# Performance work log

Hardware: AMD Instinct MI355X
Metric: run time of the kernel (lower is better)

Reference implementation:

```python
import jax, jax.numpy as jnp
import numpy as np

N_NODES = 100000
N_EDGES = 300000
D_IN = 256
D_OUT = 256


def setup_inputs() -> dict:
    key = jax.random.key(0)
    k1, k2, k3 = jax.random.split(key, 3)
    z = jax.random.normal(k1, (N_NODES, D_IN), dtype=jnp.float32)
    edge_index = jax.random.randint(k2, (2, N_EDGES), 0, N_NODES, dtype=jnp.int64)
    # Linear(input_dim, out_dim): weight [out, in], stored transposed for x @ W
    W = jax.random.normal(k3, (D_IN, D_OUT), dtype=jnp.float32) / np.sqrt(D_IN)
    b = jnp.zeros((D_OUT,), dtype=jnp.float32)
    return {"z": z, "edge_index": edge_index, "W": W, "b": b}


def reference(z, edge_index, W, b):
    # h = Linear(z): [N, D_out]
    h = z @ W + b
    # gather endpoint embeddings and take per-edge dot product
    src = h[edge_index[0]]  # [E, D_out]
    dst = h[edge_index[1]]  # [E, D_out]
    value = jnp.sum(src * dst, axis=1)  # [E]
    return jax.nn.sigmoid(value)
```

## Files before the change

kernel.cpp:

```cpp
#include <hip/hip_runtime.h>
#include <hip/hip_bf16.h>
#include <hip/hip_fp16.h>
#include <math.h>


#define D_DIM 256
#define BM 64

typedef __attribute__((ext_vector_type(8))) _Float16 half8;
typedef __attribute__((ext_vector_type(4))) float f32x4;

__device__ half8 g_Wf[8 * 256 * 4];

__global__ __launch_bounds__(256) void pack_w_kernel(const float* __restrict__ W) {
  int t = blockIdx.x * 256 + threadIdx.x;
  int kb = t >> 10;
  int qd = (t >> 8) & 3;
  int n  = t & 255;
  half8 o;
#pragma unroll
  for (int j = 0; j < 8; j++)
    o[j] = (_Float16)W[(size_t)(kb * 32 + qd * 8 + j) * D_DIM + n];
  g_Wf[(kb * 256 + n) * 4 + qd] = o;
}

__device__ inline void stage_b(int kb, char* buf, int wv, int lane) {
  const char* gsrc = (const char*)g_Wf + (size_t)kb * 16384 + wv * 2048;
  char* ldst = buf + wv * 2048;
#pragma unroll
  for (int i = 0; i < 2; i++) {
    __builtin_amdgcn_global_load_lds(
        (const __attribute__((address_space(1))) void*)(gsrc + i * 1024 + lane * 16),
        (__attribute__((address_space(3))) void*)(ldst + i * 1024),
        16, 0, 0);
  }
}

__global__ __launch_bounds__(512) void gemm_mfma_kernel(
    const float* __restrict__ z, const float* __restrict__ b,
    __half* __restrict__ h, int nrows) {
  __shared__ char smem[34816];
  const int tid = threadIdx.x;
  const int lane = tid & 63;
  const int wv = tid >> 6;
  const int mg = wv >> 1;
  const int nh = wv & 1;
  const int fr = lane & 15;
  const int qd = lane >> 4;
  const int row0 = blockIdx.x * BM + mg * 16;

  f32x4 acc[8];
#pragma unroll
  for (int j = 0; j < 8; j++) acc[j] = (f32x4)0.f;

  int r = row0 + fr;
  r = r < nrows ? r : (nrows - 1);
  const float* zrow = z + (size_t)r * D_DIM + qd * 8;

  float4 a0[2], a1[2];

  stage_b(0, smem, wv, lane);
  a0[0] = *(const float4*)(zrow);
  a1[0] = *(const float4*)(zrow + 4);
  __syncthreads();

#pragma unroll
  for (int kb = 0; kb < 8; kb++) {
    const int cA = kb & 1;
    const int nA = cA ^ 1;
    char* cur = smem + (kb & 1) * 16384;

    if (kb < 7) {
      stage_b(kb + 1, smem + ((kb + 1) & 1) * 16384, wv, lane);
      const float* p = zrow + (kb + 1) * 32;
      a0[nA] = *(const float4*)(p);
      a1[nA] = *(const float4*)(p + 4);
    }

    half8 af;
    af[0] = (_Float16)a0[cA].x; af[1] = (_Float16)a0[cA].y;
    af[2] = (_Float16)a0[cA].z; af[3] = (_Float16)a0[cA].w;
    af[4] = (_Float16)a1[cA].x; af[5] = (_Float16)a1[cA].y;
    af[6] = (_Float16)a1[cA].z; af[7] = (_Float16)a1[cA].w;

    const half8* buf = (const half8*)cur;
#pragma unroll
    for (int fn = 0; fn < 8; fn++) {
      int fi = (nh * 128 + fn * 16 + fr) * 4 + qd;
      half8 bf = buf[fi];
      acc[fn] = __builtin_amdgcn_mfma_f32_16x16x32_f16(af, bf, acc[fn], 0, 0, 0);
    }

    __syncthreads();
  }

  __half* et = (__half*)(smem + wv * 4352);
  float bias[8];
#pragma unroll
  for (int fn = 0; fn < 8; fn++) bias[fn] = b[nh * 128 + fn * 16 + fr];

#pragma unroll
  for (int fn = 0; fn < 8; fn++)
#pragma unroll
    for (int rr = 0; rr < 4; rr++)
      et[(qd * 4 + rr) * 136 + fn * 16 + fr] = __float2half(acc[fn][rr] + bias[fn]);
#pragma unroll
  for (int p = 0; p < 4; p++) {
    int idx = p * 64 + lane;
    int rr = idx >> 4;
    int cc = idx & 15;
    float4 v = *(const float4*)(et + rr * 136 + cc * 8);
    int row = row0 + rr;
    if (row < nrows)
      *(float4*)(h + (size_t)row * D_DIM + nh * 128 + cc * 8) = v;
  }
}

__global__ __launch_bounds__(256) void edge_dot_kernel(
    const int* __restrict__ ei, const __half* __restrict__ h,
    float* __restrict__ out, int E) {
  int wid = (blockIdx.x * blockDim.x + threadIdx.x) >> 6;
  int lane = threadIdx.x & 63;
  int ebase = wid * 8;
  if (ebase >= E) return;
  const int half = lane >> 5;
  const int off = lane & 31;

  float4 v[8];
#pragma unroll
  for (int q = 0; q < 8; q++) {
    int e = ebase + q;
    e = e < E ? e : (E - 1);
    int node = half ? ei[E + e] : ei[e];
    v[q] = *(const float4*)((const __half*)h + (size_t)node * D_DIM + off * 8);
  }

  float res = 0.f;
#pragma unroll
  for (int q = 0; q < 8; q++) {
    float4 w;
    w.x = __shfl_xor(v[q].x, 32);
    w.y = __shfl_xor(v[q].y, 32);
    w.z = __shfl_xor(v[q].z, 32);
    w.w = __shfl_xor(v[q].w, 32);
    const __half2* a2 = (const __half2*)&v[q];
    const __half2* b2 = (const __half2*)&w;
    float part = 0.f;
#pragma unroll
    for (int j = 0; j < 4; j++) {
      float2 fa = __half22float2(a2[j]);
      float2 fb = __half22float2(b2[j]);
      part += fa.x * fb.x + fa.y * fb.y;
    }
#pragma unroll
    for (int m = 1; m <= 16; m <<= 1) part += __shfl_xor(part, m);
    res = (lane == q) ? part : res;
  }
  if (lane < 8) {
    int e = ebase + lane;
    if (e < E) out[e] = 1.0f / (1.0f + __expf(-res));
  }
}

extern "C" void kernel_launch(void* const* d_in, const int* in_sizes, int n_in,
                              void* d_out, int out_size, void* d_ws, size_t ws_size,
                              hipStream_t stream) {
  const float* z  = (const float*)d_in[0];
  const int*   ei = (const int*)d_in[1];
  const float* W  = (const float*)d_in[2];
  const float* b  = (const float*)d_in[3];
  float* out = (float*)d_out;
  __half* h  = (__half*)d_ws;

  const int nnodes = in_sizes[0] / D_DIM;
  const int E = in_sizes[1] / 2;

  pack_w_kernel<<<32, 256, 0, stream>>>(W);

  dim3 grid_gemm((nnodes + BM - 1) / BM);
  gemm_mfma_kernel<<<grid_gemm, 512, 0, stream>>>(z, b, h, nnodes);

  int waves = (E + 7) / 8;
  dim3 grid_edge(((size_t)waves * 64 + 255) / 256);
  edge_dot_kernel<<<grid_edge, 256, 0, stream>>>(ei, h, out, E);
}
```

Baseline: 218.4 us.

## Make GEMM persistent with full W resident in LDS and per-wave row strips

The GEMM becomes a persistent kernel of 256 blocks that loads the entire packed fp16 W (128KB) into LDS once per block. Each wave then loops over 16-row strips, computing all 256 output columns with 16 accumulators and no per-k block barriers. W is repacked so each lane reads its B fragment contiguously. This removes repeated W staging and __syncthreads per k-step, at the cost of heavy LDS use (about 145KB per block), more registers, and only wave-level latency hiding for the z loads.

Measured after the change: 215.4 us. About the same (-1.4%).

```diff
diff --git a/kernel.cpp b/kernel.cpp
--- a/kernel.cpp
+++ b/kernel.cpp
@@ -5,7 +5,6 @@
 
 
 #define D_DIM 256
-#define BM 64
 
 typedef __attribute__((ext_vector_type(8))) _Float16 half8;
 typedef __attribute__((ext_vector_type(4))) float f32x4;
@@ -17,102 +16,106 @@
   int kb = t >> 10;
   int qd = (t >> 8) & 3;
   int n  = t & 255;
+  int fn = n >> 4;
+  int fr = n & 15;
   half8 o;
 #pragma unroll
   for (int j = 0; j < 8; j++)
     o[j] = (_Float16)W[(size_t)(kb * 32 + qd * 8 + j) * D_DIM + n];
-  g_Wf[(kb * 256 + n) * 4 + qd] = o;
+  g_Wf[kb * 1024 + fn * 64 + qd * 16 + fr] = o;
 }
 
-__device__ inline void stage_b(int kb, char* buf, int wv, int lane) {
-  const char* gsrc = (const char*)g_Wf + (size_t)kb * 16384 + wv * 2048;
-  char* ldst = buf + wv * 2048;
-#pragma unroll
-  for (int i = 0; i < 2; i++) {
-    __builtin_amdgcn_global_load_lds(
-        (const __attribute__((address_space(1))) void*)(gsrc + i * 1024 + lane * 16),
-        (__attribute__((address_space(3))) void*)(ldst + i * 1024),
-        16, 0, 0);
-  }
-}
-
-__global__ __launch_bounds__(512) void gemm_mfma_kernel(
+__global__ __launch_bounds__(512, 2) void gemm_mfma_kernel(
     const float* __restrict__ z, const float* __restrict__ b,
     __half* __restrict__ h, int nrows) {
-  __shared__ char smem[34816];
+  __shared__ char smem[131072 + 8 * 2176];
   const int tid = threadIdx.x;
   const int lane = tid & 63;
   const int wv = tid >> 6;
-  const int mg = wv >> 1;
-  const int nh = wv & 1;
   const int fr = lane & 15;
   const int qd = lane >> 4;
-  const int row0 = blockIdx.x * BM + mg * 16;
 
-  f32x4 acc[8];
+  {
+    const char* gsrc = (const char*)g_Wf;
 #pragma unroll
-  for (int j = 0; j < 8; j++) acc[j] = (f32x4)0.f;
+    for (int rnd = 0; rnd < 16; rnd++) {
+      int off = rnd * 8192 + wv * 1024;
+      __builtin_amdgcn_global_load_lds(
+          (const __attribute__((address_space(1))) void*)(gsrc + off + lane * 16),
+          (__attribute__((address_space(3))) void*)(smem + off),
+          16, 0, 0);
+    }
+  }
+  float bias[16];
+#pragma unroll
+  for (int fn = 0; fn < 16; fn++) bias[fn] = b[fn * 16 + fr];
 
-  int r = row0 + fr;
-  r = r < nrows ? r : (nrows - 1);
-  const float* zrow = z + (size_t)r * D_DIM + qd * 8;
-
-  float4 a0[2], a1[2];
-
-  stage_b(0, smem, wv, lane);
-  a0[0] = *(const float4*)(zrow);
-  a1[0] = *(const float4*)(zrow + 4);
   __syncthreads();
 
+  const half8* bw = (const half8*)smem;
+  __half* et = (__half*)(smem + 131072 + wv * 2176);
+
+  const int gw = blockIdx.x * 8 + wv;
+  const int nstrips = (nrows + 15) >> 4;
+
+#pragma unroll 1
+  for (int s = gw; s < nstrips; s += 2048) {
+    int r = s * 16 + fr;
+    r = r < nrows ? r : (nrows - 1);
+    const float* zr = z + (size_t)r * D_DIM + qd * 8;
+
+    float4 a0[8], a1[8];
 #pragma unroll
-  for (int kb = 0; kb < 8; kb++) {
-    const int cA = kb & 1;
-    const int nA = cA ^ 1;
-    char* cur = smem + (kb & 1) * 16384;
+    for (int kb = 0; kb < 8; kb++) {
+      a0[kb] = *(const float4*)(zr + kb * 32);
+      a1[kb] = *(const float4*)(zr + kb * 32 + 4);
+    }
+    asm volatile("" ::: "memory");
 
-    if (kb < 7) {
-      stage_b(kb + 1, smem + ((kb + 1) & 1) * 16384, wv, lane);
-      const float* p = zrow + (kb + 1) * 32;
-      a0[nA] = *(const float4*)(p);
-      a1[nA] = *(const float4*)(p + 4);
+    f32x4 acc[16];
+#pragma unroll
+    for (int fn = 0; fn < 16; fn++) acc[fn] = (f32x4)0.f;
+
+#pragma unroll
+    for (int kb = 0; kb < 8; kb++) {
+      half8 af;
+      af[0] = (_Float16)a0[kb].x; af[1] = (_Float16)a0[kb].y;
+      af[2] = (_Float16)a0[kb].z; af[3] = (_Float16)a0[kb].w;
+      af[4] = (_Float16)a1[kb].x; af[5] = (_Float16)a1[kb].y;
+      af[6] = (_Float16)a1[kb].z; af[7] = (_Float16)a1[kb].w;
+#pragma unroll
+      for (int fn = 0; fn < 16; fn++) {
+        half8 bf = bw[kb * 1024 + fn * 64 + lane];
+        acc[fn] = __builtin_amdgcn_mfma_f32_16x16x32_f16(af, bf, acc[fn], 0, 0, 0);
+      }
     }
 
-    half8 af;
-    af[0] = (_Float16)a0[cA].x; af[1] = (_Float16)a0[cA].y;
-    af[2] = (_Float16)a0[cA].z; af[3] = (_Float16)a0[cA].w;
-    af[4] = (_Float16)a1[cA].x; af[5] = (_Float16)a1[cA].y;
-    af[6] = (_Float16)a1[cA].z; af[7] = (_Float16)a1[cA].w;
-
-    const half8* buf = (const half8*)cur;
 #pragma unroll
-    for (int fn = 0; fn < 8; fn++) {
-      int fi = (nh * 128 + fn * 16 + fr) * 4 + qd;
-      half8 bf = buf[fi];
-      acc[fn] = __builtin_amdgcn_mfma_f32_16x16x32_f16(af, bf, acc[fn], 0, 0, 0);
+    for (int ph = 0; ph < 2; ph++) {
+#pragma unroll
+      for (int ch = 0; ch < 2; ch++) {
+        if ((qd >> 1) == ph) {
+#pragma unroll
+          for (int f2 = 0; f2 < 8; f2++) {
+            int fn = ch * 8 + f2;
+#pragma unroll
+            for (int rr = 0; rr < 4; rr++)
+              et[((qd & 1) * 4 + rr) * 136 + f2 * 16 + fr] =
+                  __float2half(acc[fn][rr] + bias[fn]);
+          }
+        }
+#pragma unroll
+        for (int p = 0; p < 2; p++) {
+          int idx = p * 64 + lane;
+          int rr = idx >> 4;
+          int cc = idx & 15;
+          float4 v = *(const float4*)(et + rr * 136 + cc * 8);
+          int row = s * 16 + ph * 8 + rr;
+          if (row < nrows)
+            *(float4*)(h + (size_t)row * D_DIM + ch * 128 + cc * 8) = v;
+        }
+      }
     }
-
-    __syncthreads();
-  }
-
-  __half* et = (__half*)(smem + wv * 4352);
-  float bias[8];
-#pragma unroll
-  for (int fn = 0; fn < 8; fn++) bias[fn] = b[nh * 128 + fn * 16 + fr];
-
-#pragma unroll
-  for (int fn = 0; fn < 8; fn++)
-#pragma unroll
-    for (int rr = 0; rr < 4; rr++)
-      et[(qd * 4 + rr) * 136 + fn * 16 + fr] = __float2half(acc[fn][rr] + bias[fn]);
-#pragma unroll
-  for (int p = 0; p < 4; p++) {
-    int idx = p * 64 + lane;
-    int rr = idx >> 4;
-    int cc = idx & 15;
-    float4 v = *(const float4*)(et + rr * 136 + cc * 8);
-    int row = row0 + rr;
-    if (row < nrows)
-      *(float4*)(h + (size_t)row * D_DIM + nh * 128 + cc * 8) = v;
   }
 }
 
@@ -177,8 +180,7 @@
 
   pack_w_kernel<<<32, 256, 0, stream>>>(W);
 
-  dim3 grid_gemm((nnodes + BM - 1) / BM);
-  gemm_mfma_kernel<<<grid_gemm, 512, 0, stream>>>(z, b, h, nnodes);
+  gemm_mfma_kernel<<<256, 512, 0, stream>>>(z, b, h, nnodes);
 
   int waves = (E + 7) / 8;
   dim3 grid_edge(((size_t)waves * 64 + 255) / 256);
```
